# Optimization experiments

Hardware: AMD Instinct MI355X
Metric: run time of the kernel (lower is better)

## Reference

```python
import jax, jax.numpy as jnp
import numpy as np

N, E, IN, H, D = 100000, 1600000, 128, 4, 64
NEG_SLOPE = 0.2
K_APPNP, ALPHA = 5, 0.5
BN_EPS = 1e-5


def setup_inputs() -> dict:
    key = jax.random.key(0)
    ks = jax.random.split(key, 12)
    return {
        'node_feats': jax.random.normal(ks[0], (N, IN), jnp.float32),
        'src': jax.random.randint(ks[1], (E,), 0, N, jnp.int32),
        'dst': jax.random.randint(ks[2], (E,), 0, N, jnp.int32),
        'W_fc': jax.random.normal(ks[3], (IN, H * D), jnp.float32) * (1.0 / np.sqrt(IN)),
        'attn_l': jax.random.normal(ks[4], (H, D), jnp.float32) * 0.1,
        'attn_r': jax.random.normal(ks[5], (H, D), jnp.float32) * 0.1,
        'W_res_gat': jax.random.normal(ks[6], (IN, H * D), jnp.float32) * (1.0 / np.sqrt(IN)),
        'gat_bias': jax.random.normal(ks[7], (H * D,), jnp.float32) * 0.01,
        'conv_w': jax.random.normal(ks[8], (1, H), jnp.float32) * 0.5,
        'conv_b': jax.random.normal(ks[9], (1,), jnp.float32) * 0.01,
        'W_res': jax.random.normal(ks[10], (D, IN), jnp.float32) * (1.0 / np.sqrt(IN)),
        'b_res': jax.random.normal(ks[11], (D,), jnp.float32) * 0.01,
        'gamma': jnp.ones((D,), jnp.float32),
        'beta': jnp.zeros((D,), jnp.float32),
    }


def reference(node_feats, src, dst, W_fc, attn_l, attn_r, W_res_gat, gat_bias,
              conv_w, conv_b, W_res, b_res, gamma, beta):
    # ---- GATConv (4 heads, residual, relu) ----
    feat = (node_feats @ W_fc).reshape(N, H, D)            # (N,H,D)
    el = jnp.einsum('nhd,hd->nh', feat, attn_l)            # (N,H)
    er = jnp.einsum('nhd,hd->nh', feat, attn_r)
    e = jax.nn.leaky_relu(el[src] + er[dst], NEG_SLOPE)    # (E,H)
    # edge softmax over incoming edges of each dst node
    emax = jax.ops.segment_max(e, dst, num_segments=N)     # (N,H)
    emax = jnp.where(jnp.isfinite(emax), emax, 0.0)
    ee = jnp.exp(e - emax[dst])                            # (E,H)
    denom = jax.ops.segment_sum(ee, dst, num_segments=N)   # (N,H)
    a = ee / jnp.maximum(denom[dst], 1e-9)                 # (E,H)
    msg = feat[src] * a[..., None]                         # (E,H,D)
    rst = jax.ops.segment_sum(msg, dst, num_segments=N)    # (N,H,D)
    resval = (node_feats @ W_res_gat).reshape(N, H, D)
    rst = jax.nn.relu(rst + resval + gat_bias.reshape(1, H, D))
    # ---- Conv1d (heads -> 1, kernel_size=1) then flatten ----
    h = jnp.einsum('nhd,oh->nod', rst, conv_w) + conv_b[None, :, None]
    h = h.reshape(N, D)
    # ---- APPNP (k=5, alpha=0.5), symmetric deg^{-1/2} norm (in-degree, clamp 1) ----
    deg = jax.ops.segment_sum(jnp.ones((E,), jnp.float32), dst, num_segments=N)
    norm = jnp.power(jnp.maximum(deg, 1.0), -0.5)[:, None]  # (N,1)
    h0 = h
    for _ in range(K_APPNP):
        h = jax.ops.segment_sum((h * norm)[src], dst, num_segments=N) * norm
        h = (1.0 - ALPHA) * h + ALPHA * h0
    # ---- residual linear + relu ----
    h = h + jax.nn.relu(node_feats @ W_res.T + b_res)
    # ---- BatchNorm1d (batch stats, affine) ----
    mu = h.mean(axis=0)
    var = h.var(axis=0)
    return (h - mu) * jax.lax.rsqrt(var + BN_EPS) * gamma + beta
```

## Files before the change

kernel.cpp:

```cpp
#include <hip/hip_runtime.h>
#include <math.h>

#define NN 100000
#define NE 1600000
#define NEG_SLOPE 0.2f

typedef __attribute__((ext_vector_type(8))) short bf16x8;
typedef __attribute__((ext_vector_type(4))) float f32x4;

__device__ __forceinline__ float b2f(unsigned short u) {
  union { unsigned u; float f; } c; c.u = ((unsigned)u) << 16; return c.f;
}
__device__ __forceinline__ unsigned short f2b(float x) {
  union { float f; unsigned u; } c; c.f = x;
  unsigned r = c.u + 0x7FFFu + ((c.u >> 16) & 1u);
  return (unsigned short)(r >> 16);
}
__device__ __forceinline__ float wred(float v) {
#pragma unroll
  for (int off = 32; off > 0; off >>= 1) v += __shfl_xor(v, off, 64);
  return v;
}
__device__ __forceinline__ float readlane_f(float v, int l) {
  return __uint_as_float((unsigned)__builtin_amdgcn_readlane((int)__float_as_uint(v), l));
}
__device__ __forceinline__ void fma4(float4& acc, float s, const float4& b) {
  acc.x = fmaf(s, b.x, acc.x);
  acc.y = fmaf(s, b.y, acc.y);
  acc.z = fmaf(s, b.z, acc.z);
  acc.w = fmaf(s, b.w, acc.w);
}

__global__ __launch_bounds__(256) void k_zero(int* __restrict__ p, int nwords) {
  int i = blockIdx.x * 256 + threadIdx.x;
  if (i < nwords) p[i] = 0;
}

__global__ void k_zrow(unsigned short* __restrict__ a, unsigned short* __restrict__ b) {
  int i = threadIdx.x;
  a[(size_t)NN * 64 + i] = 0;
  b[(size_t)NN * 64 + i] = 0;
}

__global__ __launch_bounds__(256) void k_cast(const float* __restrict__ A, unsigned short* __restrict__ Ab) {
  int i = blockIdx.x * 256 + threadIdx.x;
  int i4 = i * 4;
  if (i4 < NN * 128) {
    float4 v = *(const float4*)&A[i4];
    ushort4 o; o.x = f2b(v.x); o.y = f2b(v.y); o.z = f2b(v.z); o.w = f2b(v.w);
    *(ushort4*)&Ab[i4] = o;
  }
}

__global__ __launch_bounds__(256) void k_deg(const int* __restrict__ dst, int* __restrict__ deg) {
  int i = blockIdx.x * 256 + threadIdx.x;
  if (i < NE) atomicAdd(&deg[dst[i]], 1);
}

__global__ __launch_bounds__(256) void k_alloc(const int* __restrict__ deg, int* __restrict__ row_start,
                                               int* __restrict__ counter, float* __restrict__ nrm) {
  int i = blockIdx.x * 256 + threadIdx.x;
  if (i < NN) {
    row_start[i] = atomicAdd(counter, deg[i]);
    nrm[i] = rsqrtf(fmaxf((float)deg[i], 1.0f));
  }
}

__global__ __launch_bounds__(256) void k_scatter(const int* __restrict__ src, const int* __restrict__ dst,
                                                 const int* __restrict__ row_start, int* __restrict__ cursor,
                                                 int* __restrict__ csr_src) {
  int i = blockIdx.x * 256 + threadIdx.x;
  if (i < NE) {
    int n = dst[i];
    int p = atomicAdd(&cursor[n], 1);
    csr_src[row_start[n] + p] = src[i];
  }
}

__global__ __launch_bounds__(256) void k_prepB(const float* __restrict__ W_fc, const float* __restrict__ W_rg,
                                               unsigned short* __restrict__ Bp) {
  int y = blockIdx.y;
  const float* Bsrc = (y >> 1) ? W_rg : W_fc;
  int colbase = (y & 1) * 128;
  for (int e = blockIdx.x * 256 + threadIdx.x; e < 16384; e += 2048) {
    int n = e & 127, k = e >> 7;
    int p = colbase + n;
    int d = p >> 2, hh = p & 3;
    float v = Bsrc[k * 256 + hh * 64 + d];
    int nt = n >> 4, nn = n & 15, kt = k >> 5, quad = (k >> 3) & 3, j = k & 7;
    Bp[(size_t)y * 16384 + ((nt * 4 + kt) * 64 + quad * 16 + nn) * 8 + j] = f2b(v);
  }
}

__global__ __launch_bounds__(256) void k_gemm_mfma(const unsigned short* __restrict__ Abf,
                                                   const unsigned short* __restrict__ Bp,
                                                   unsigned short* __restrict__ feat2,
                                                   unsigned short* __restrict__ resval2) {
  __shared__ unsigned short Bl[16384];
  int tid = threadIdx.x;
  unsigned short* Cdst = (blockIdx.y >> 1) ? resval2 : feat2;
  int colbase = (blockIdx.y & 1) * 128;
  {
    const uint4* src = (const uint4*)(Bp + (size_t)blockIdx.y * 16384);
    uint4* dst4 = (uint4*)Bl;
#pragma unroll
    for (int i = 0; i < 8; ++i) dst4[tid + i * 256] = src[tid + i * 256];
  }
  __syncthreads();
  int w = tid >> 6, lane = tid & 63;
  int quad = lane >> 4;
  int row0 = blockIdx.x * 128;
  int mrow = row0 + (lane & 15);
  f32x4 acc[8][2];
#pragma unroll
  for (int rt = 0; rt < 8; ++rt)
#pragma unroll
    for (int c = 0; c < 2; ++c) acc[rt][c] = (f32x4){0.f, 0.f, 0.f, 0.f};
#pragma unroll
  for (int kt = 0; kt < 4; ++kt) {
    bf16x8 b0 = *(const bf16x8*)&Bl[(((w * 2 + 0) * 4 + kt) * 64 + lane) * 8];
    bf16x8 b1 = *(const bf16x8*)&Bl[(((w * 2 + 1) * 4 + kt) * 64 + lane) * 8];
    int kb = kt * 32 + quad * 8;
#pragma unroll
    for (int rt = 0; rt < 8; ++rt) {
      int rr = mrow + rt * 16; if (rr > NN - 1) rr = NN - 1;
      bf16x8 a = *(const bf16x8*)&Abf[(size_t)rr * 128 + kb];
      acc[rt][0] = __builtin_amdgcn_mfma_f32_16x16x32_bf16(b0, a, acc[rt][0], 0, 0, 0);
      acc[rt][1] = __builtin_amdgcn_mfma_f32_16x16x32_bf16(b1, a, acc[rt][1], 0, 0, 0);
    }
  }
#pragma unroll
  for (int rt = 0; rt < 8; ++rt) {
    int m = row0 + rt * 16 + (lane & 15);
    if (m < NN) {
#pragma unroll
      for (int c = 0; c < 2; ++c) {
        int col = colbase + (w * 2 + c) * 16 + quad * 4;
        ushort4 o;
        o.x = f2b(acc[rt][c][0]); o.y = f2b(acc[rt][c][1]);
        o.z = f2b(acc[rt][c][2]); o.w = f2b(acc[rt][c][3]);
        *(ushort4*)&Cdst[(size_t)m * 256 + col] = o;
      }
    }
  }
}

__global__ __launch_bounds__(256) void k_gemm_nt_bias_relu(const float* __restrict__ A, const float* __restrict__ B,
                                                           const float* __restrict__ bias, float* __restrict__ C) {
  __shared__ float Bl[128][68];
  for (int idx = threadIdx.x; idx < 64 * 128; idx += 256) {
    int d = idx >> 7, k = idx & 127;
    Bl[k][d] = B[d * 128 + k];
  }
  __syncthreads();
  int tx = threadIdx.x & 15, ty = threadIdx.x >> 4;
  int row0 = blockIdx.x * 64 + ty * 4;
  const float* ap[4];
#pragma unroll
  for (int r = 0; r < 4; ++r) ap[r] = A + (size_t)min(row0 + r, NN - 1) * 128;
  float4 acc[4];
#pragma unroll
  for (int r = 0; r < 4; ++r) acc[r] = make_float4(0.f, 0.f, 0.f, 0.f);
#pragma unroll 2
  for (int k0 = 0; k0 < 128; k0 += 4) {
    float4 b0 = *(const float4*)&Bl[k0][tx * 4];
    float4 b1 = *(const float4*)&Bl[k0 + 1][tx * 4];
    float4 b2 = *(const float4*)&Bl[k0 + 2][tx * 4];
    float4 b3 = *(const float4*)&Bl[k0 + 3][tx * 4];
#pragma unroll
    for (int r = 0; r < 4; ++r) {
      float4 a = *(const float4*)(ap[r] + k0);
      fma4(acc[r], a.x, b0); fma4(acc[r], a.y, b1);
      fma4(acc[r], a.z, b2); fma4(acc[r], a.w, b3);
    }
  }
  float4 bv = *(const float4*)&bias[tx * 4];
#pragma unroll
  for (int r = 0; r < 4; ++r) {
    int row = row0 + r;
    if (row < NN) {
      float4 v;
      v.x = fmaxf(acc[r].x + bv.x, 0.f);
      v.y = fmaxf(acc[r].y + bv.y, 0.f);
      v.z = fmaxf(acc[r].z + bv.z, 0.f);
      v.w = fmaxf(acc[r].w + bv.w, 0.f);
      *(float4*)&C[(size_t)row * 64 + tx * 4] = v;
    }
  }
}

__global__ __launch_bounds__(256) void k_elr(const unsigned short* __restrict__ feat2, const float* __restrict__ al,
                                             const float* __restrict__ ar, float* __restrict__ el,
                                             float* __restrict__ er) {
  int n = blockIdx.x * 4 + (threadIdx.x >> 6);
  int lane = threadIdx.x & 63;
  if (n >= NN) return;
  ushort4 v = *(const ushort4*)&feat2[(size_t)n * 256 + lane * 4];
  float v0 = b2f(v.x), v1 = b2f(v.y), v2 = b2f(v.z), v3 = b2f(v.w);
  float l0 = wred(v0 * al[lane]);       float r0 = wred(v0 * ar[lane]);
  float l1 = wred(v1 * al[64 + lane]);  float r1 = wred(v1 * ar[64 + lane]);
  float l2 = wred(v2 * al[128 + lane]); float r2 = wred(v2 * ar[128 + lane]);
  float l3 = wred(v3 * al[192 + lane]); float r3 = wred(v3 * ar[192 + lane]);
  if (lane == 0) {
    *(float4*)&el[n * 4] = make_float4(l0, l1, l2, l3);
    *(float4*)&er[n * 4] = make_float4(r0, r1, r2, r3);
  }
}

__global__ __launch_bounds__(256) void k_gat(const int* __restrict__ row_start, const int* __restrict__ deg,
                                             const int* __restrict__ csr_src, const float* __restrict__ el,
                                             const float* __restrict__ er, const unsigned short* __restrict__ feat2,
                                             const unsigned short* __restrict__ resval2,
                                             const float* __restrict__ gat_bias, const float* __restrict__ conv_w,
                                             const float* __restrict__ conv_b, const float* __restrict__ nrm,
                                             float* __restrict__ h0, unsigned short* __restrict__ hsA) {
  int n = blockIdx.x * 4 + (threadIdx.x >> 6);
  int lane = threadIdx.x & 63;
  if (n >= NN) return;
  int s0 = row_start[n], cnt = deg[n];
  float4 er4 = *(const float4*)&er[n * 4];
  float acc0 = 0.f, acc1 = 0.f, acc2 = 0.f, acc3 = 0.f;
  float den0 = 0.f, den1 = 0.f, den2 = 0.f, den3 = 0.f;
  for (int base = 0; base < cnt; base += 64) {
    int j = base + lane;
    int s = 0;
    float x0 = 0.f, x1 = 0.f, x2 = 0.f, x3 = 0.f;
    if (j < cnt) {
      s = csr_src[s0 + j];
      float4 el4 = *(const float4*)&el[s * 4];
      float e0 = el4.x + er4.x; e0 = (e0 > 0.f) ? e0 : NEG_SLOPE * e0;
      float e1 = el4.y + er4.y; e1 = (e1 > 0.f) ? e1 : NEG_SLOPE * e1;
      float e2 = el4.z + er4.z; e2 = (e2 > 0.f) ? e2 : NEG_SLOPE * e2;
      float e3 = el4.w + er4.w; e3 = (e3 > 0.f) ? e3 : NEG_SLOPE * e3;
      x0 = __expf(e0); x1 = __expf(e1); x2 = __expf(e2); x3 = __expf(e3);
      den0 += x0; den1 += x1; den2 += x2; den3 += x3;
    }
    int m = cnt - base; if (m > 64) m = 64;
    int mr = (m + 3) & ~3;
    for (int t = 0; t < mr; t += 4) {
      int ss0 = __builtin_amdgcn_readlane(s, t);
      int ss1 = __builtin_amdgcn_readlane(s, t + 1);
      int ss2 = __builtin_amdgcn_readlane(s, t + 2);
      int ss3 = __builtin_amdgcn_readlane(s, t + 3);
      uint2 f0 = *(const uint2*)&feat2[(size_t)ss0 * 256 + lane * 4];
      uint2 f1 = *(const uint2*)&feat2[(size_t)ss1 * 256 + lane * 4];
      uint2 f2 = *(const uint2*)&feat2[(size_t)ss2 * 256 + lane * 4];
      uint2 f3 = *(const uint2*)&feat2[(size_t)ss3 * 256 + lane * 4];
      float a00 = readlane_f(x0, t),     a10 = readlane_f(x1, t),     a20 = readlane_f(x2, t),     a30 = readlane_f(x3, t);
      float a01 = readlane_f(x0, t + 1), a11 = readlane_f(x1, t + 1), a21 = readlane_f(x2, t + 1), a31 = readlane_f(x3, t + 1);
      float a02 = readlane_f(x0, t + 2), a12 = readlane_f(x1, t + 2), a22 = readlane_f(x2, t + 2), a32 = readlane_f(x3, t + 2);
      float a03 = readlane_f(x0, t + 3), a13 = readlane_f(x1, t + 3), a23 = readlane_f(x2, t + 3), a33 = readlane_f(x3, t + 3);
      acc0 = fmaf(a00, __uint_as_float(f0.x << 16), acc0);
      acc1 = fmaf(a10, __uint_as_float(f0.x & 0xffff0000u), acc1);
      acc2 = fmaf(a20, __uint_as_float(f0.y << 16), acc2);
      acc3 = fmaf(a30, __uint_as_float(f0.y & 0xffff0000u), acc3);
      acc0 = fmaf(a01, __uint_as_float(f1.x << 16), acc0);
      acc1 = fmaf(a11, __uint_as_float(f1.x & 0xffff0000u), acc1);
      acc2 = fmaf(a21, __uint_as_float(f1.y << 16), acc2);
      acc3 = fmaf(a31, __uint_as_float(f1.y & 0xffff0000u), acc3);
      acc0 = fmaf(a02, __uint_as_float(f2.x << 16), acc0);
      acc1 = fmaf(a12, __uint_as_float(f2.x & 0xffff0000u), acc1);
      acc2 = fmaf(a22, __uint_as_float(f2.y << 16), acc2);
      acc3 = fmaf(a32, __uint_as_float(f2.y & 0xffff0000u), acc3);
      acc0 = fmaf(a03, __uint_as_float(f3.x << 16), acc0);
      acc1 = fmaf(a13, __uint_as_float(f3.x & 0xffff0000u), acc1);
      acc2 = fmaf(a23, __uint_as_float(f3.y << 16), acc2);
      acc3 = fmaf(a33, __uint_as_float(f3.y & 0xffff0000u), acc3);
    }
  }
  den0 = wred(den0); den1 = wred(den1); den2 = wred(den2); den3 = wred(den3);
  float i0 = 1.f / fmaxf(den0, 1e-9f);
  float i1 = 1.f / fmaxf(den1, 1e-9f);
  float i2 = 1.f / fmaxf(den2, 1e-9f);
  float i3 = 1.f / fmaxf(den3, 1e-9f);
  ushort4 rv = *(const ushort4*)&resval2[(size_t)n * 256 + lane * 4];
  float hmix = conv_b[0];
  float t0;
  t0 = fmaf(acc0, i0, b2f(rv.x) + gat_bias[lane]);       t0 = fmaxf(t0, 0.f); hmix = fmaf(conv_w[0], t0, hmix);
  t0 = fmaf(acc1, i1, b2f(rv.y) + gat_bias[64 + lane]);  t0 = fmaxf(t0, 0.f); hmix = fmaf(conv_w[1], t0, hmix);
  t0 = fmaf(acc2, i2, b2f(rv.z) + gat_bias[128 + lane]); t0 = fmaxf(t0, 0.f); hmix = fmaf(conv_w[2], t0, hmix);
  t0 = fmaf(acc3, i3, b2f(rv.w) + gat_bias[192 + lane]); t0 = fmaxf(t0, 0.f); hmix = fmaf(conv_w[3], t0, hmix);
  size_t o = (size_t)n * 64 + lane;
  h0[o] = hmix;
  hsA[o] = f2b(hmix * nrm[n]);
}

__global__ __launch_bounds__(256) void k_gather_mid(const int* __restrict__ row_start, const int* __restrict__ deg,
                                                    const int* __restrict__ csr_src,
                                                    const unsigned short* __restrict__ hs_in,
                                                    const float* __restrict__ nrm, const float* __restrict__ h0,
                                                    unsigned short* __restrict__ hs_out) {
  int n = blockIdx.x * 4 + (threadIdx.x >> 6);
  int lane = threadIdx.x & 63;
  if (n >= NN) return;
  int s0 = row_start[n], cnt = deg[n];
  float acc = 0.f;
  for (int base = 0; base < cnt; base += 64) {
    int j = base + lane;
    int s = (j < cnt) ? csr_src[s0 + j] : NN;
    int m = cnt - base; if (m > 64) m = 64;
    int mr = (m + 3) & ~3;
    for (int t = 0; t < mr; t += 4) {
      int ss0 = __builtin_amdgcn_readlane(s, t);
      int ss1 = __builtin_amdgcn_readlane(s, t + 1);
      int ss2 = __builtin_amdgcn_readlane(s, t + 2);
      int ss3 = __builtin_amdgcn_readlane(s, t + 3);
      float u0 = b2f(hs_in[(size_t)ss0 * 64 + lane]);
      float u1 = b2f(hs_in[(size_t)ss1 * 64 + lane]);
      float u2 = b2f(hs_in[(size_t)ss2 * 64 + lane]);
      float u3 = b2f(hs_in[(size_t)ss3 * 64 + lane]);
      acc += (u0 + u1) + (u2 + u3);
    }
  }
  size_t o = (size_t)n * 64 + lane;
  float nn_ = nrm[n];
  float v = fmaf(0.5f * nn_, acc, 0.5f * h0[o]);
  hs_out[o] = f2b(v * nn_);
}

__global__ __launch_bounds__(256) void k_gather_last(const int* __restrict__ row_start, const int* __restrict__ deg,
                                                     const int* __restrict__ csr_src,
                                                     const unsigned short* __restrict__ hs_in,
                                                     const float* __restrict__ nrm, const float* __restrict__ h0,
                                                     unsigned short* __restrict__ hout) {
  int n = blockIdx.x * 4 + (threadIdx.x >> 6);
  int lane = threadIdx.x & 63;
  if (n >= NN) return;
  int s0 = row_start[n], cnt = deg[n];
  float acc = 0.f;
  for (int base = 0; base < cnt; base += 64) {
    int j = base + lane;
    int s = (j < cnt) ? csr_src[s0 + j] : NN;
    int m = cnt - base; if (m > 64) m = 64;
    int mr = (m + 3) & ~3;
    for (int t = 0; t < mr; t += 4) {
      int ss0 = __builtin_amdgcn_readlane(s, t);
      int ss1 = __builtin_amdgcn_readlane(s, t + 1);
      int ss2 = __builtin_amdgcn_readlane(s, t + 2);
      int ss3 = __builtin_amdgcn_readlane(s, t + 3);
      float u0 = b2f(hs_in[(size_t)ss0 * 64 + lane]);
      float u1 = b2f(hs_in[(size_t)ss1 * 64 + lane]);
      float u2 = b2f(hs_in[(size_t)ss2 * 64 + lane]);
      float u3 = b2f(hs_in[(size_t)ss3 * 64 + lane]);
      acc += (u0 + u1) + (u2 + u3);
    }
  }
  size_t o = (size_t)n * 64 + lane;
  float v = fmaf(0.5f * nrm[n], acc, 0.5f * h0[o]);
  hout[o] = f2b(v);
}

__global__ __launch_bounds__(256) void k_finred(const unsigned short* __restrict__ hl,
                                                const float* __restrict__ res2, float* __restrict__ hfin,
                                                float* __restrict__ bn) {
  __shared__ float s1[256], s2[256];
  int d = threadIdx.x & 63;
  int rb = blockIdx.x * 64;
  float sum = 0.f, sq = 0.f;
  for (int r = threadIdx.x >> 6; r < 64; r += 4) {
    int n = rb + r;
    if (n < NN) {
      size_t idx = (size_t)n * 64 + d;
      float v = b2f(hl[idx]) + res2[idx];
      hfin[idx] = v;
      sum += v; sq += v * v;
    }
  }
  s1[threadIdx.x] = sum; s2[threadIdx.x] = sq;
  __syncthreads();
  if (threadIdx.x < 128) { s1[threadIdx.x] += s1[threadIdx.x + 128]; s2[threadIdx.x] += s2[threadIdx.x + 128]; }
  __syncthreads();
  if (threadIdx.x < 64) {
    atomicAdd(&bn[d], s1[threadIdx.x] + s1[threadIdx.x + 64]);
    atomicAdd(&bn[64 + d], s2[threadIdx.x] + s2[threadIdx.x + 64]);
  }
}

__global__ void k_bnstats(const float* __restrict__ bn, const float* __restrict__ gamma,
                          const float* __restrict__ beta, float* __restrict__ bns) {
  int d = threadIdx.x;
  float mu = bn[d] * (1.0f / NN);
  float var = fmaxf(bn[64 + d] * (1.0f / NN) - mu * mu, 0.f);
  float sc = rsqrtf(var + 1e-5f) * gamma[d];
  bns[d] = sc;
  bns[64 + d] = beta[d] - mu * sc;
}

__global__ __launch_bounds__(256) void k_bnapply(const float* __restrict__ h, const float* __restrict__ bns,
                                                 float* __restrict__ out) {
  int i = blockIdx.x * 256 + threadIdx.x;
  if (i < NN * 64) {
    int d = i & 63;
    out[i] = fmaf(h[i], bns[d], bns[64 + d]);
  }
}

extern "C" void kernel_launch(void* const* d_in, const int* in_sizes, int n_in,
                              void* d_out, int out_size, void* d_ws, size_t ws_size,
                              hipStream_t stream) {
  const float* node_feats = (const float*)d_in[0];
  const int* src = (const int*)d_in[1];
  const int* dst = (const int*)d_in[2];
  const float* W_fc = (const float*)d_in[3];
  const float* attn_l = (const float*)d_in[4];
  const float* attn_r = (const float*)d_in[5];
  const float* W_res_gat = (const float*)d_in[6];
  const float* gat_bias = (const float*)d_in[7];
  const float* conv_w = (const float*)d_in[8];
  const float* conv_b = (const float*)d_in[9];
  const float* W_res = (const float*)d_in[10];
  const float* b_res = (const float*)d_in[11];
  const float* gamma = (const float*)d_in[12];
  const float* beta = (const float*)d_in[13];
  float* out = (float*)d_out;

  char* base = (char*)d_ws;
  size_t off = 0;
  auto alloc = [&](size_t bytes) -> char* {
    char* p = base + off;
    off = (off + bytes + 255) & ~(size_t)255;
    return p;
  };
  unsigned short* feat2   = (unsigned short*)alloc((size_t)NN * 256 * 2);
  unsigned short* resval2 = (unsigned short*)alloc((size_t)NN * 256 * 2);
  float* res2             = (float*)resval2;
  float* el               = (float*)alloc((size_t)NN * 4 * 4);
  float* er               = (float*)alloc((size_t)NN * 4 * 4);
  float* h0               = (float*)alloc((size_t)NN * 64 * 4);
  unsigned short* Abf     = (unsigned short*)h0;
  unsigned short* hsA     = (unsigned short*)alloc((size_t)(NN + 1) * 64 * 2);
  unsigned short* hsB     = (unsigned short*)alloc((size_t)(NN + 1) * 64 * 2);
  unsigned short* hout    = hsB;
  int* csr_src            = (int*)alloc((size_t)NE * 4);
  float* nrm              = (float*)alloc((size_t)NN * 4);
  int* row_start          = (int*)alloc((size_t)NN * 4);
  unsigned short* Bpacked = (unsigned short*)alloc((size_t)4 * 16384 * 2);
  size_t zoff = off;
  int* deg                = (int*)alloc((size_t)NN * 4);
  int* cursor             = (int*)alloc((size_t)NN * 4);
  int* counter            = (int*)alloc(256);
  float* bn               = (float*)alloc(256 * 4);
  float* hfin             = h0;

  int zwords = (int)((off - zoff) / 4);
  int gE = (NE + 255) / 256;
  int gN = (NN + 255) / 256;
  int gW = (NN + 3) / 4;
  int gM = (NN + 63) / 64;
  int gV = (NN * 64 + 255) / 256;

  k_zero<<<(zwords + 255) / 256, 256, 0, stream>>>((int*)(base + zoff), zwords);
  k_zrow<<<1, 64, 0, stream>>>(hsA, hsB);
  k_deg<<<gE, 256, 0, stream>>>(dst, deg);
  k_alloc<<<gN, 256, 0, stream>>>(deg, row_start, counter, nrm);
  k_scatter<<<gE, 256, 0, stream>>>(src, dst, row_start, cursor, csr_src);

  k_cast<<<(NN * 128 / 4 + 255) / 256, 256, 0, stream>>>(node_feats, Abf);
  k_prepB<<<dim3(8, 4), 256, 0, stream>>>(W_fc, W_res_gat, Bpacked);
  k_gemm_mfma<<<dim3((NN + 127) / 128, 4), 256, 0, stream>>>(Abf, Bpacked, feat2, resval2);

  k_elr<<<gW, 256, 0, stream>>>(feat2, attn_l, attn_r, el, er);
  k_gat<<<gW, 256, 0, stream>>>(row_start, deg, csr_src, el, er, feat2, resval2,
                                gat_bias, conv_w, conv_b, nrm, h0, hsA);

  k_gemm_nt_bias_relu<<<gM, 256, 0, stream>>>(node_feats, W_res, b_res, res2);

  k_gather_mid<<<gW, 256, 0, stream>>>(row_start, deg, csr_src, hsA, nrm, h0, hsB);
  k_gather_mid<<<gW, 256, 0, stream>>>(row_start, deg, csr_src, hsB, nrm, h0, hsA);
  k_gather_mid<<<gW, 256, 0, stream>>>(row_start, deg, csr_src, hsA, nrm, h0, hsB);
  k_gather_mid<<<gW, 256, 0, stream>>>(row_start, deg, csr_src, hsB, nrm, h0, hsA);
  k_gather_last<<<gW, 256, 0, stream>>>(row_start, deg, csr_src, hsA, nrm, h0, hout);

  k_finred<<<gM, 256, 0, stream>>>(hout, res2, hfin, bn);
  k_bnstats<<<1, 64, 0, stream>>>(bn, gamma, beta, bn + 128);
  k_bnapply<<<gV, 256, 0, stream>>>(hfin, bn + 128, out);
}
```

Baseline: 907.8 us.

## Store GAT features in fp8, fold attention into weights, unroll APPNP gathers

The projected GAT features are now stored as packed fp8 instead of bf16, which halves the bytes moved by the edge gather in the attention aggregation; accumulation uses packed f32x2 math. The el/er attention scores are now computed from the fp32 inputs through precomputed W_fc·attn vectors, so k_elr no longer reads the full feature matrix. The APPNP gather loops issue eight neighbour loads per step instead of four. fp8 quantization of the features adds approximation error that may challenge tolerance, and the final output gets its own buffer.

```diff
diff --git a/kernel.cpp b/kernel.cpp
--- a/kernel.cpp
+++ b/kernel.cpp
@@ -7,6 +7,7 @@
 
 typedef __attribute__((ext_vector_type(8))) short bf16x8;
 typedef __attribute__((ext_vector_type(4))) float f32x4;
+typedef __attribute__((ext_vector_type(2))) float f32x2;
 
 __device__ __forceinline__ float b2f(unsigned short u) {
   union { unsigned u; float f; } c; c.u = ((unsigned)u) << 16; return c.f;
@@ -15,11 +16,6 @@
   union { float f; unsigned u; } c; c.f = x;
   unsigned r = c.u + 0x7FFFu + ((c.u >> 16) & 1u);
   return (unsigned short)(r >> 16);
-}
-__device__ __forceinline__ float wred(float v) {
-#pragma unroll
-  for (int off = 32; off > 0; off >>= 1) v += __shfl_xor(v, off, 64);
-  return v;
 }
 __device__ __forceinline__ float readlane_f(float v, int l) {
   return __uint_as_float((unsigned)__builtin_amdgcn_readlane((int)__float_as_uint(v), l));
@@ -29,6 +25,11 @@
   acc.y = fmaf(s, b.y, acc.y);
   acc.z = fmaf(s, b.z, acc.z);
   acc.w = fmaf(s, b.w, acc.w);
+}
+__device__ __forceinline__ float wred(float v) {
+#pragma unroll
+  for (int off = 32; off > 0; off >>= 1) v += __shfl_xor(v, off, 64);
+  return v;
 }
 
 __global__ __launch_bounds__(256) void k_zero(int* __restrict__ p, int nwords) {
@@ -75,6 +76,36 @@
     int p = atomicAdd(&cursor[n], 1);
     csr_src[row_start[n] + p] = src[i];
   }
+}
+
+__global__ __launch_bounds__(256) void k_prepw(const float* __restrict__ W_fc, const float* __restrict__ al,
+                                               const float* __restrict__ ar, float* __restrict__ w) {
+  int o = blockIdx.x * 256 + threadIdx.x;
+  if (o >= 1024) return;
+  int side = o >> 9;
+  int h = (o >> 7) & 3;
+  int k = o & 127;
+  const float* a = side ? ar : al;
+  float s = 0.f;
+  for (int d = 0; d < 64; ++d) s += W_fc[k * 256 + h * 64 + d] * a[h * 64 + d];
+  w[(side * 4 + h) * 128 + k] = s;
+}
+
+__global__ __launch_bounds__(256) void k_elr2(const float* __restrict__ X, const float* __restrict__ w,
+                                              float* __restrict__ el, float* __restrict__ er) {
+  int n = blockIdx.x * 32 + (threadIdx.x >> 3);
+  int p = threadIdx.x & 7;
+  if (n >= NN) return;
+  const float4* xr = (const float4*)(X + (size_t)n * 128);
+  const float4* wr = (const float4*)(w + p * 128);
+  float s = 0.f;
+#pragma unroll
+  for (int i = 0; i < 32; ++i) {
+    float4 x = xr[i], ww = wr[i];
+    s += x.x * ww.x + x.y * ww.y + x.z * ww.z + x.w * ww.w;
+  }
+  if (p < 4) el[n * 4 + p] = s;
+  else er[n * 4 + (p - 4)] = s;
 }
 
 __global__ __launch_bounds__(256) void k_prepB(const float* __restrict__ W_fc, const float* __restrict__ W_rg,
@@ -94,11 +125,11 @@
 
 __global__ __launch_bounds__(256) void k_gemm_mfma(const unsigned short* __restrict__ Abf,
                                                    const unsigned short* __restrict__ Bp,
-                                                   unsigned short* __restrict__ feat2,
+                                                   unsigned* __restrict__ feat8u,
                                                    unsigned short* __restrict__ resval2) {
   __shared__ unsigned short Bl[16384];
   int tid = threadIdx.x;
-  unsigned short* Cdst = (blockIdx.y >> 1) ? resval2 : feat2;
+  int half = blockIdx.y >> 1;
   int colbase = (blockIdx.y & 1) * 128;
   {
     const uint4* src = (const uint4*)(Bp + (size_t)blockIdx.y * 16384);
@@ -136,10 +167,16 @@
 #pragma unroll
       for (int c = 0; c < 2; ++c) {
         int col = colbase + (w * 2 + c) * 16 + quad * 4;
-        ushort4 o;
-        o.x = f2b(acc[rt][c][0]); o.y = f2b(acc[rt][c][1]);
-        o.z = f2b(acc[rt][c][2]); o.w = f2b(acc[rt][c][3]);
-        *(ushort4*)&Cdst[(size_t)m * 256 + col] = o;
+        if (half == 0) {
+          int pk = __builtin_amdgcn_cvt_pk_fp8_f32(acc[rt][c][0], acc[rt][c][1], 0, false);
+          pk = __builtin_amdgcn_cvt_pk_fp8_f32(acc[rt][c][2], acc[rt][c][3], pk, true);
+          feat8u[(size_t)m * 64 + (col >> 2)] = (unsigned)pk;
+        } else {
+          ushort4 o;
+          o.x = f2b(acc[rt][c][0]); o.y = f2b(acc[rt][c][1]);
+          o.z = f2b(acc[rt][c][2]); o.w = f2b(acc[rt][c][3]);
+          *(ushort4*)&resval2[(size_t)m * 256 + col] = o;
+        }
       }
     }
   }
@@ -189,27 +226,9 @@
   }
 }
 
-__global__ __launch_bounds__(256) void k_elr(const unsigned short* __restrict__ feat2, const float* __restrict__ al,
-                                             const float* __restrict__ ar, float* __restrict__ el,
-                                             float* __restrict__ er) {
-  int n = blockIdx.x * 4 + (threadIdx.x >> 6);
-  int lane = threadIdx.x & 63;
-  if (n >= NN) return;
-  ushort4 v = *(const ushort4*)&feat2[(size_t)n * 256 + lane * 4];
-  float v0 = b2f(v.x), v1 = b2f(v.y), v2 = b2f(v.z), v3 = b2f(v.w);
-  float l0 = wred(v0 * al[lane]);       float r0 = wred(v0 * ar[lane]);
-  float l1 = wred(v1 * al[64 + lane]);  float r1 = wred(v1 * ar[64 + lane]);
-  float l2 = wred(v2 * al[128 + lane]); float r2 = wred(v2 * ar[128 + lane]);
-  float l3 = wred(v3 * al[192 + lane]); float r3 = wred(v3 * ar[192 + lane]);
-  if (lane == 0) {
-    *(float4*)&el[n * 4] = make_float4(l0, l1, l2, l3);
-    *(float4*)&er[n * 4] = make_float4(r0, r1, r2, r3);
-  }
-}
-
 __global__ __launch_bounds__(256) void k_gat(const int* __restrict__ row_start, const int* __restrict__ deg,
                                              const int* __restrict__ csr_src, const float* __restrict__ el,
-                                             const float* __restrict__ er, const unsigned short* __restrict__ feat2,
+                                             const float* __restrict__ er, const unsigned* __restrict__ feat8u,
                                              const unsigned short* __restrict__ resval2,
                                              const float* __restrict__ gat_bias, const float* __restrict__ conv_w,
                                              const float* __restrict__ conv_b, const float* __restrict__ nrm,
@@ -219,7 +238,7 @@
   if (n >= NN) return;
   int s0 = row_start[n], cnt = deg[n];
   float4 er4 = *(const float4*)&er[n * 4];
-  float acc0 = 0.f, acc1 = 0.f, acc2 = 0.f, acc3 = 0.f;
+  f32x2 acc01 = (f32x2){0.f, 0.f}, acc23 = (f32x2){0.f, 0.f};
   float den0 = 0.f, den1 = 0.f, den2 = 0.f, den3 = 0.f;
   for (int base = 0; base < cnt; base += 64) {
     int j = base + lane;
@@ -242,30 +261,38 @@
       int ss1 = __builtin_amdgcn_readlane(s, t + 1);
       int ss2 = __builtin_amdgcn_readlane(s, t + 2);
       int ss3 = __builtin_amdgcn_readlane(s, t + 3);
-      uint2 f0 = *(const uint2*)&feat2[(size_t)ss0 * 256 + lane * 4];
-      uint2 f1 = *(const uint2*)&feat2[(size_t)ss1 * 256 + lane * 4];
-      uint2 f2 = *(const uint2*)&feat2[(size_t)ss2 * 256 + lane * 4];
-      uint2 f3 = *(const uint2*)&feat2[(size_t)ss3 * 256 + lane * 4];
-      float a00 = readlane_f(x0, t),     a10 = readlane_f(x1, t),     a20 = readlane_f(x2, t),     a30 = readlane_f(x3, t);
-      float a01 = readlane_f(x0, t + 1), a11 = readlane_f(x1, t + 1), a21 = readlane_f(x2, t + 1), a31 = readlane_f(x3, t + 1);
-      float a02 = readlane_f(x0, t + 2), a12 = readlane_f(x1, t + 2), a22 = readlane_f(x2, t + 2), a32 = readlane_f(x3, t + 2);
-      float a03 = readlane_f(x0, t + 3), a13 = readlane_f(x1, t + 3), a23 = readlane_f(x2, t + 3), a33 = readlane_f(x3, t + 3);
-      acc0 = fmaf(a00, __uint_as_float(f0.x << 16), acc0);
-      acc1 = fmaf(a10, __uint_as_float(f0.x & 0xffff0000u), acc1);
-      acc2 = fmaf(a20, __uint_as_float(f0.y << 16), acc2);
-      acc3 = fmaf(a30, __uint_as_float(f0.y & 0xffff0000u), acc3);
-      acc0 = fmaf(a01, __uint_as_float(f1.x << 16), acc0);
-      acc1 = fmaf(a11, __uint_as_float(f1.x & 0xffff0000u), acc1);
-      acc2 = fmaf(a21, __uint_as_float(f1.y << 16), acc2);
-      acc3 = fmaf(a31, __uint_as_float(f1.y & 0xffff0000u), acc3);
-      acc0 = fmaf(a02, __uint_as_float(f2.x << 16), acc0);
-      acc1 = fmaf(a12, __uint_as_float(f2.x & 0xffff0000u), acc1);
-      acc2 = fmaf(a22, __uint_as_float(f2.y << 16), acc2);
-      acc3 = fmaf(a32, __uint_as_float(f2.y & 0xffff0000u), acc3);
-      acc0 = fmaf(a03, __uint_as_float(f3.x << 16), acc0);
-      acc1 = fmaf(a13, __uint_as_float(f3.x & 0xffff0000u), acc1);
-      acc2 = fmaf(a23, __uint_as_float(f3.y << 16), acc2);
-      acc3 = fmaf(a33, __uint_as_float(f3.y & 0xffff0000u), acc3);
+      unsigned f0 = feat8u[(size_t)ss0 * 64 + lane];
+      unsigned f1 = feat8u[(size_t)ss1 * 64 + lane];
+      unsigned f2 = feat8u[(size_t)ss2 * 64 + lane];
+      unsigned f3 = feat8u[(size_t)ss3 * 64 + lane];
+      {
+        f32x2 a01 = (f32x2){readlane_f(x0, t), readlane_f(x1, t)};
+        f32x2 a23 = (f32x2){readlane_f(x2, t), readlane_f(x3, t)};
+        f32x2 lo = __builtin_amdgcn_cvt_pk_f32_fp8((int)f0, false);
+        f32x2 hi = __builtin_amdgcn_cvt_pk_f32_fp8((int)f0, true);
+        acc01 += a01 * lo; acc23 += a23 * hi;
+      }
+      {
+        f32x2 a01 = (f32x2){readlane_f(x0, t + 1), readlane_f(x1, t + 1)};
+        f32x2 a23 = (f32x2){readlane_f(x2, t + 1), readlane_f(x3, t + 1)};
+        f32x2 lo = __builtin_amdgcn_cvt_pk_f32_fp8((int)f1, false);
+        f32x2 hi = __builtin_amdgcn_cvt_pk_f32_fp8((int)f1, true);
+        acc01 += a01 * lo; acc23 += a23 * hi;
+      }
+      {
+        f32x2 a01 = (f32x2){readlane_f(x0, t + 2), readlane_f(x1, t + 2)};
+        f32x2 a23 = (f32x2){readlane_f(x2, t + 2), readlane_f(x3, t + 2)};
+        f32x2 lo = __builtin_amdgcn_cvt_pk_f32_fp8((int)f2, false);
+        f32x2 hi = __builtin_amdgcn_cvt_pk_f32_fp8((int)f2, true);
+        acc01 += a01 * lo; acc23 += a23 * hi;
+      }
+      {
+        f32x2 a01 = (f32x2){readlane_f(x0, t + 3), readlane_f(x1, t + 3)};
+        f32x2 a23 = (f32x2){readlane_f(x2, t + 3), readlane_f(x3, t + 3)};
+        f32x2 lo = __builtin_amdgcn_cvt_pk_f32_fp8((int)f3, false);
+        f32x2 hi = __builtin_amdgcn_cvt_pk_f32_fp8((int)f3, true);
+        acc01 += a01 * lo; acc23 += a23 * hi;
+      }
     }
   }
   den0 = wred(den0); den1 = wred(den1); den2 = wred(den2); den3 = wred(den3);
@@ -276,10 +303,10 @@
   ushort4 rv = *(const ushort4*)&resval2[(size_t)n * 256 + lane * 4];
   float hmix = conv_b[0];
   float t0;
-  t0 = fmaf(acc0, i0, b2f(rv.x) + gat_bias[lane]);       t0 = fmaxf(t0, 0.f); hmix = fmaf(conv_w[0], t0, hmix);
-  t0 = fmaf(acc1, i1, b2f(rv.y) + gat_bias[64 + lane]);  t0 = fmaxf(t0, 0.f); hmix = fmaf(conv_w[1], t0, hmix);
-  t0 = fmaf(acc2, i2, b2f(rv.z) + gat_bias[128 + lane]); t0 = fmaxf(t0, 0.f); hmix = fmaf(conv_w[2], t0, hmix);
-  t0 = fmaf(acc3, i3, b2f(rv.w) + gat_bias[192 + lane]); t0 = fmaxf(t0, 0.f); hmix = fmaf(conv_w[3], t0, hmix);
+  t0 = fmaf(acc01.x, i0, b2f(rv.x) + gat_bias[lane]);       t0 = fmaxf(t0, 0.f); hmix = fmaf(conv_w[0], t0, hmix);
+  t0 = fmaf(acc01.y, i1, b2f(rv.y) + gat_bias[64 + lane]);  t0 = fmaxf(t0, 0.f); hmix = fmaf(conv_w[1], t0, hmix);
+  t0 = fmaf(acc23.x, i2, b2f(rv.z) + gat_bias[128 + lane]); t0 = fmaxf(t0, 0.f); hmix = fmaf(conv_w[2], t0, hmix);
+  t0 = fmaf(acc23.y, i3, b2f(rv.w) + gat_bias[192 + lane]); t0 = fmaxf(t0, 0.f); hmix = fmaf(conv_w[3], t0, hmix);
   size_t o = (size_t)n * 64 + lane;
   h0[o] = hmix;
   hsA[o] = f2b(hmix * nrm[n]);
@@ -299,17 +326,25 @@
     int j = base + lane;
     int s = (j < cnt) ? csr_src[s0 + j] : NN;
     int m = cnt - base; if (m > 64) m = 64;
-    int mr = (m + 3) & ~3;
-    for (int t = 0; t < mr; t += 4) {
+    int mr = (m + 7) & ~7;
+    for (int t = 0; t < mr; t += 8) {
       int ss0 = __builtin_amdgcn_readlane(s, t);
       int ss1 = __builtin_amdgcn_readlane(s, t + 1);
       int ss2 = __builtin_amdgcn_readlane(s, t + 2);
       int ss3 = __builtin_amdgcn_readlane(s, t + 3);
+      int ss4 = __builtin_amdgcn_readlane(s, t + 4);
+      int ss5 = __builtin_amdgcn_readlane(s, t + 5);
+      int ss6 = __builtin_amdgcn_readlane(s, t + 6);
+      int ss7 = __builtin_amdgcn_readlane(s, t + 7);
       float u0 = b2f(hs_in[(size_t)ss0 * 64 + lane]);
       float u1 = b2f(hs_in[(size_t)ss1 * 64 + lane]);
       float u2 = b2f(hs_in[(size_t)ss2 * 64 + lane]);
       float u3 = b2f(hs_in[(size_t)ss3 * 64 + lane]);
-      acc += (u0 + u1) + (u2 + u3);
+      float u4 = b2f(hs_in[(size_t)ss4 * 64 + lane]);
+      float u5 = b2f(hs_in[(size_t)ss5 * 64 + lane]);
+      float u6 = b2f(hs_in[(size_t)ss6 * 64 + lane]);
+      float u7 = b2f(hs_in[(size_t)ss7 * 64 + lane]);
+      acc += ((u0 + u1) + (u2 + u3)) + ((u4 + u5) + (u6 + u7));
     }
   }
   size_t o = (size_t)n * 64 + lane;
@@ -332,17 +367,25 @@
     int j = base + lane;
     int s = (j < cnt) ? csr_src[s0 + j] : NN;
     int m = cnt - base; if (m > 64) m = 64;
-    int mr = (m + 3) & ~3;
-    for (int t = 0; t < mr; t += 4) {
+    int mr = (m + 7) & ~7;
+    for (int t = 0; t < mr; t += 8) {
       int ss0 = __builtin_amdgcn_readlane(s, t);
       int ss1 = __builtin_amdgcn_readlane(s, t + 1);
       int ss2 = __builtin_amdgcn_readlane(s, t + 2);
       int ss3 = __builtin_amdgcn_readlane(s, t + 3);
+      int ss4 = __builtin_amdgcn_readlane(s, t + 4);
+      int ss5 = __builtin_amdgcn_readlane(s, t + 5);
+      int ss6 = __builtin_amdgcn_readlane(s, t + 6);
+      int ss7 = __builtin_amdgcn_readlane(s, t + 7);
       float u0 = b2f(hs_in[(size_t)ss0 * 64 + lane]);
       float u1 = b2f(hs_in[(size_t)ss1 * 64 + lane]);
       float u2 = b2f(hs_in[(size_t)ss2 * 64 + lane]);
       float u3 = b2f(hs_in[(size_t)ss3 * 64 + lane]);
-      acc += (u0 + u1) + (u2 + u3);
+      float u4 = b2f(hs_in[(size_t)ss4 * 64 + lane]);
+      float u5 = b2f(hs_in[(size_t)ss5 * 64 + lane]);
+      float u6 = b2f(hs_in[(size_t)ss6 * 64 + lane]);
+      float u7 = b2f(hs_in[(size_t)ss7 * 64 + lane]);
+      acc += ((u0 + u1) + (u2 + u3)) + ((u4 + u5) + (u6 + u7));
     }
   }
   size_t o = (size_t)n * 64 + lane;
@@ -421,7 +464,7 @@
     off = (off + bytes + 255) & ~(size_t)255;
     return p;
   };
-  unsigned short* feat2   = (unsigned short*)alloc((size_t)NN * 256 * 2);
+  unsigned* feat8u        = (unsigned*)alloc((size_t)NN * 256);
   unsigned short* resval2 = (unsigned short*)alloc((size_t)NN * 256 * 2);
   float* res2             = (float*)resval2;
   float* el               = (float*)alloc((size_t)NN * 4 * 4);
@@ -430,11 +473,12 @@
   unsigned short* Abf     = (unsigned short*)h0;
   unsigned short* hsA     = (unsigned short*)alloc((size_t)(NN + 1) * 64 * 2);
   unsigned short* hsB     = (unsigned short*)alloc((size_t)(NN + 1) * 64 * 2);
-  unsigned short* hout    = hsB;
+  unsigned short* hout    = (unsigned short*)alloc((size_t)NN * 64 * 2);
   int* csr_src            = (int*)alloc((size_t)NE * 4);
   float* nrm              = (float*)alloc((size_t)NN * 4);
   int* row_start          = (int*)alloc((size_t)NN * 4);
   unsigned short* Bpacked = (unsigned short*)alloc((size_t)4 * 16384 * 2);
+  float* w_elr            = (float*)alloc((size_t)8 * 128 * 4);
   size_t zoff = off;
   int* deg                = (int*)alloc((size_t)NN * 4);
   int* cursor             = (int*)alloc((size_t)NN * 4);
@@ -457,10 +501,11 @@
 
   k_cast<<<(NN * 128 / 4 + 255) / 256, 256, 0, stream>>>(node_feats, Abf);
   k_prepB<<<dim3(8, 4), 256, 0, stream>>>(W_fc, W_res_gat, Bpacked);
-  k_gemm_mfma<<<dim3((NN + 127) / 128, 4), 256, 0, stream>>>(Abf, Bpacked, feat2, resval2);
-
-  k_elr<<<gW, 256, 0, stream>>>(feat2, attn_l, attn_r, el, er);
-  k_gat<<<gW, 256, 0, stream>>>(row_start, deg, csr_src, el, er, feat2, resval2,
+  k_prepw<<<4, 256, 0, stream>>>(W_fc, attn_l, attn_r, w_elr);
+  k_gemm_mfma<<<dim3((NN + 127) / 128, 4), 256, 0, stream>>>(Abf, Bpacked, feat8u, resval2);
+
+  k_elr2<<<(NN + 31) / 32, 256, 0, stream>>>(node_feats, w_elr, el, er);
+  k_gat<<<gW, 256, 0, stream>>>(row_start, deg, csr_src, el, er, feat8u, resval2,
                                 gat_bias, conv_w, conv_b, nrm, h0, hsA);
 
   k_gemm_nt_bias_relu<<<gM, 256, 0, stream>>>(node_feats, W_res, b_res, res2);
```

New measurement: 843.2 us. -7.1%, faster.
